# Kernel tuning notes

Hardware: AMD Instinct MI355X
Metric: run time of the kernel (lower is better)

The kernel has to match this reference:

```python
import jax, jax.numpy as jnp
import numpy as np

DIM = 1024
N_HEADS = 16
HEAD_DIM = DIM // N_HEADS


def setup_inputs() -> dict:
    key = jax.random.key(0)
    ks = jax.random.split(key, 5)
    B, L = 2, 2048
    q = jax.random.normal(ks[0], (B, L, DIM), dtype=jnp.float32)
    # nn.Linear weights: shape [out_features, in_features], applied as x @ W.T
    scale = 1.0 / np.sqrt(DIM)
    Wq = jax.random.normal(ks[1], (DIM, DIM), dtype=jnp.float32) * scale
    Wk = jax.random.normal(ks[2], (DIM, DIM), dtype=jnp.float32) * scale
    Wv = jax.random.normal(ks[3], (DIM, DIM), dtype=jnp.float32) * scale
    Wo = jax.random.normal(ks[4], (DIM, DIM), dtype=jnp.float32) * scale
    return {"q": q, "Wq": Wq, "Wk": Wk, "Wv": Wv, "Wo": Wo}


def reference(q, Wq, Wk, Wv, Wo):
    B, L, _ = q.shape
    kv = q  # self-attention (kv=None path)
    # projections: x @ W.T, then split heads: b l (h d) -> b h l d
    def split_heads(x):
        return x.reshape(B, L, N_HEADS, HEAD_DIM).transpose(0, 2, 1, 3)
    qh = split_heads(q @ Wq.T)
    kh = split_heads(kv @ Wk.T)
    vh = split_heads(kv @ Wv.T)
    # scaled dot-product attention; scale = sqrt(head_dim)
    scores = jnp.einsum('bhid,bhjd->bhij', qh, kh) / jnp.sqrt(
        jnp.asarray(HEAD_DIM, dtype=qh.dtype))
    attn = jax.nn.softmax(scores, axis=-1)
    out = jnp.einsum('bhij,bhjd->bhid', attn, vh)
    # b h l d -> b l (h d)
    out = out.transpose(0, 2, 1, 3).reshape(B, L, DIM)
    return out @ Wo.T
```

## Files before the change

kernel.cpp:

```cpp
#include <hip/hip_runtime.h>


#define DIMN 1024
#define NH 16
#define HD 64
#define BB 2
#define LL 2048

typedef float f32x4 __attribute__((ext_vector_type(4)));
typedef short s16x8 __attribute__((ext_vector_type(8)));

#define QSCALE 0.18033688011112042f

static __device__ __forceinline__ unsigned short f2bf(float f) {
  unsigned u = __float_as_uint(f);
  u += 0x7fffu + ((u >> 16) & 1u);
  return (unsigned short)(u >> 16);
}
static __device__ __forceinline__ unsigned packbf2(float lo, float hi) {
  return (unsigned)f2bf(lo) | ((unsigned)f2bf(hi) << 16);
}
static __device__ __forceinline__ float xexp2(float x) {
#if __has_builtin(__builtin_amdgcn_exp2f)
  return __builtin_amdgcn_exp2f(x);
#else
  return exp2f(x);
#endif
}
static __device__ __forceinline__ s16x8 cvt8(float4 a, float4 b) {
  s16x8 r;
  r[0] = (short)f2bf(a.x); r[1] = (short)f2bf(a.y);
  r[2] = (short)f2bf(a.z); r[3] = (short)f2bf(a.w);
  r[4] = (short)f2bf(b.x); r[5] = (short)f2bf(b.y);
  r[6] = (short)f2bf(b.z); r[7] = (short)f2bf(b.w);
  return r;
}
static __device__ __forceinline__ void gld16(const unsigned short* g,
                                             unsigned short* l) {
#if __has_builtin(__builtin_amdgcn_global_load_lds)
  __builtin_amdgcn_global_load_lds(
      (const __attribute__((address_space(1))) void*)g,
      (__attribute__((address_space(3))) void*)l, 16, 0, 0);
#else
  ((uint4*)l)[threadIdx.x & 63] = ((const uint4*)g)[0];
#endif
}

static __device__ __forceinline__ int vpos(int s128) {
  return (s128 & 0x60) | ((s128 & 0x0C) << 1) | ((s128 & 0x10) >> 2) | (s128 & 3);
}

__global__ __launch_bounds__(256) void cvt_all(
    const float* __restrict__ X, const float* __restrict__ Wq,
    const float* __restrict__ Wk, const float* __restrict__ Wv,
    const float* __restrict__ Wo, unsigned short* __restrict__ out) {
  const int blk = blockIdx.x;
  const float* src;
  unsigned short* dst;
  size_t off;
  if (blk < 2048) {
    src = X; dst = out; off = (size_t)blk * 2048;
  } else {
    int s = (blk - 2048) >> 9;
    src = (s == 0) ? Wq : (s == 1) ? Wk : (s == 2) ? Wv : Wo;
    dst = out + ((size_t)1 << 22) + (size_t)s * (1u << 20);
    off = (size_t)((blk - 2048) & 511) * 2048;
  }
  size_t i = off + (size_t)threadIdx.x * 8;
  float4 v0 = *(const float4*)(src + i);
  float4 v1 = *(const float4*)(src + i + 4);
  uint4 o;
  o.x = packbf2(v0.x, v0.y); o.y = packbf2(v0.z, v0.w);
  o.z = packbf2(v1.x, v1.y); o.w = packbf2(v1.z, v1.w);
  *(uint4*)(dst + i) = o;
}

__global__ __launch_bounds__(256) void gemm_qkv(
    const unsigned short* __restrict__ Xb, const unsigned short* __restrict__ Wb,
    unsigned short* __restrict__ Qb, unsigned short* __restrict__ Kb,
    unsigned short* __restrict__ VT) {
  __shared__ __align__(16) unsigned short Al[128 * 32];
  __shared__ __align__(16) unsigned short Bl[128 * 32];
  const int m0 = blockIdx.x * 128;
  const int n0g = blockIdx.y * 128;
  const int sel = n0g >> 10;
  const int tid = threadIdx.x;
  const int w = tid >> 6, lane = tid & 63;
  const int c = lane & 15, quad = lane >> 4;
  const int wm = (w & 1) * 64, wn = (w >> 1) * 64;

  f32x4 zero = {0.f, 0.f, 0.f, 0.f};
  f32x4 acc[4][4];
#pragma unroll
  for (int i = 0; i < 4; ++i)
#pragma unroll
    for (int j = 0; j < 4; ++j) acc[i][j] = zero;

  const int srow = w * 32 + (lane >> 2);
  const int scol = (lane & 3) * 8;
  const unsigned short* gA = Xb + (size_t)(m0 + srow) * DIMN + scol;
  const unsigned short* gB = Wb + (size_t)(n0g + srow) * DIMN + scol;
  unsigned short* lA0 = Al + (w * 32) * 32;
  unsigned short* lA1 = Al + (w * 32 + 16) * 32;
  unsigned short* lB0 = Bl + (w * 32) * 32;
  unsigned short* lB1 = Bl + (w * 32 + 16) * 32;

  for (int k0 = 0; k0 < DIMN; k0 += 32) {
    __syncthreads();
    gld16(gA + k0, lA0);
    gld16(gA + k0 + 16 * DIMN, lA1);
    gld16(gB + k0, lB0);
    gld16(gB + k0 + 16 * DIMN, lB1);
    __syncthreads();
    s16x8 a[4], b[4];
#pragma unroll
    for (int i = 0; i < 4; ++i)
      a[i] = *(const s16x8*)&Al[(wm + i * 16 + c) * 32 + quad * 8];
#pragma unroll
    for (int j = 0; j < 4; ++j)
      b[j] = *(const s16x8*)&Bl[(wn + j * 16 + c) * 32 + quad * 8];
    if (sel != 2) {
#pragma unroll
      for (int i = 0; i < 4; ++i)
#pragma unroll
        for (int j = 0; j < 4; ++j)
          acc[i][j] = __builtin_amdgcn_mfma_f32_16x16x32_bf16(a[i], b[j], acc[i][j], 0, 0, 0);
    } else {
#pragma unroll
      for (int i = 0; i < 4; ++i)
#pragma unroll
        for (int j = 0; j < 4; ++j)
          acc[i][j] = __builtin_amdgcn_mfma_f32_16x16x32_bf16(b[j], a[i], acc[i][j], 0, 0, 0);
    }
  }

  const int n0 = n0g & 1023;
  if (sel != 2) {
    unsigned short* Out = (sel == 0) ? Qb : Kb;
    const float scale = (sel == 0) ? QSCALE : 1.0f;
#pragma unroll
    for (int i = 0; i < 4; ++i)
#pragma unroll
      for (int j = 0; j < 4; ++j)
#pragma unroll
        for (int r = 0; r < 4; ++r) {
          int row = m0 + wm + i * 16 + quad * 4 + r;
          int col = n0 + wn + j * 16 + c;
          Out[(((size_t)(row >> 11) * NH + (col >> 6)) * LL + (row & 2047)) * HD + (col & 63)] =
              f2bf(acc[i][j][r] * scale);
        }
  } else {
#pragma unroll
    for (int i = 0; i < 4; ++i) {
#pragma unroll
      for (int j = 0; j < 4; ++j)
#pragma unroll
        for (int r = 0; r < 4; ++r) {
          int n = n0 + wn + j * 16 + quad * 4 + r;
          int sp = vpos(wm + i * 16 + c);
          int m = m0 + sp;
          int bi = (m0 + wm) >> 11;
          VT[(((size_t)bi * NH + (n >> 6)) * HD + (n & 63)) * LL + (m & 2047)] =
              f2bf(acc[i][j][r]);
        }
    }
  }
}

__global__ __launch_bounds__(256) void gemm_o(
    const unsigned short* __restrict__ A, const unsigned short* __restrict__ Wob,
    float* __restrict__ Out) {
  __shared__ __align__(16) unsigned short Al[128 * 32];
  __shared__ __align__(16) unsigned short Bl[64 * 32];
  const int m0 = blockIdx.x * 128;
  const int n0 = blockIdx.y * 64;
  const int tid = threadIdx.x;
  const int w = tid >> 6, lane = tid & 63;
  const int c = lane & 15, quad = lane >> 4;
  const int wm = (w & 1) * 64, wn = (w >> 1) * 32;

  f32x4 zero = {0.f, 0.f, 0.f, 0.f};
  f32x4 acc[4][2];
#pragma unroll
  for (int i = 0; i < 4; ++i)
#pragma unroll
    for (int j = 0; j < 2; ++j) acc[i][j] = zero;

  const int srow = w * 32 + (lane >> 2);
  const int brow = w * 16 + (lane >> 2);
  const int scol = (lane & 3) * 8;
  const unsigned short* gA = A + (size_t)(m0 + srow) * DIMN + scol;
  const unsigned short* gB = Wob + (size_t)(n0 + brow) * DIMN + scol;
  unsigned short* lA0 = Al + (w * 32) * 32;
  unsigned short* lA1 = Al + (w * 32 + 16) * 32;
  unsigned short* lB0 = Bl + (w * 16) * 32;

  for (int k0 = 0; k0 < DIMN; k0 += 32) {
    __syncthreads();
    gld16(gA + k0, lA0);
    gld16(gA + k0 + 16 * DIMN, lA1);
    gld16(gB + k0, lB0);
    __syncthreads();
    s16x8 a[4], b[2];
#pragma unroll
    for (int i = 0; i < 4; ++i)
      a[i] = *(const s16x8*)&Al[(wm + i * 16 + c) * 32 + quad * 8];
#pragma unroll
    for (int j = 0; j < 2; ++j)
      b[j] = *(const s16x8*)&Bl[(wn + j * 16 + c) * 32 + quad * 8];
#pragma unroll
    for (int i = 0; i < 4; ++i)
#pragma unroll
      for (int j = 0; j < 2; ++j)
        acc[i][j] = __builtin_amdgcn_mfma_f32_16x16x32_bf16(a[i], b[j], acc[i][j], 0, 0, 0);
  }

#pragma unroll
  for (int i = 0; i < 4; ++i)
#pragma unroll
    for (int j = 0; j < 2; ++j)
#pragma unroll
      for (int r = 0; r < 4; ++r)
        Out[(size_t)(m0 + wm + i * 16 + quad * 4 + r) * DIMN + n0 + wn + j * 16 + c] =
            acc[i][j][r];
}

__global__ __launch_bounds__(512) void attn6(
    const unsigned short* __restrict__ Qb, const unsigned short* __restrict__ Kb,
    const unsigned short* __restrict__ VT, unsigned short* __restrict__ AO) {
  __shared__ __align__(16) unsigned short Kl[2 * 128 * 64];
  __shared__ __align__(16) unsigned short Vtl[2 * 64 * 128];

  const int bh = blockIdx.y;
  const int tid = threadIdx.x;
  const int w = tid >> 6, lane = tid & 63;
  const int c = lane & 15, quad = lane >> 4;
  const int q0 = blockIdx.x * 128 + w * 16;

  const unsigned short* Qh = Qb + (size_t)bh * LL * HD;
  const unsigned short* Kh = Kb + (size_t)bh * LL * HD;
  const unsigned short* Vh = VT + (size_t)bh * HD * LL;

  s16x8 qf0 = *(const s16x8*)(Qh + (size_t)(q0 + c) * HD + quad * 8);
  s16x8 qf1 = *(const s16x8*)(Qh + (size_t)(q0 + c) * HD + 32 + quad * 8);

  f32x4 zero = {0.f, 0.f, 0.f, 0.f};
  f32x4 o[4];
  float lsum = 0.f;
#pragma unroll
  for (int dc = 0; dc < 4; ++dc) o[dc] = zero;

  const int l8 = lane >> 3, p8 = lane & 7;
  const unsigned short* gK = Kh + (size_t)(w * 16 + l8) * HD + ((p8 ^ l8) * 8);
  const int l16 = lane >> 4, p16 = lane & 15;
  const int vr0 = w * 8 + l16;
  const int vr1 = w * 8 + 4 + l16;
  const unsigned short* gV0 = Vh + (size_t)vr0 * LL + ((p16 ^ (vr0 & 15)) * 8);
  const unsigned short* gV1 = Vh + (size_t)vr1 * LL + ((p16 ^ (vr1 & 15)) * 8);

  const int kpa = (quad ^ (c & 7)) * 8;
  const int kpb = ((quad + 4) ^ (c & 7)) * 8;

#define STAGE(buf, k0)                                                        \
  do {                                                                        \
    unsigned short* lK_ = Kl + (buf) * (128 * 64) + (w * 16) * 64;            \
    unsigned short* lV_ = Vtl + (buf) * (64 * 128) + (w * 8) * 128;           \
    gld16(gK + (size_t)(k0) * HD, lK_);                                       \
    gld16(gK + (size_t)((k0) + 8) * HD, lK_ + 8 * 64);                        \
    gld16(gV0 + (k0), lV_);                                                   \
    gld16(gV1 + (k0), lV_ + 4 * 128);                                         \
  } while (0)

  STAGE(0, 0);

  for (int it = 0; it < LL / 128; ++it) {
    __syncthreads();
    if (it + 1 < LL / 128) STAGE((it + 1) & 1, (it + 1) * 128);
    const unsigned short* Kt = Kl + (it & 1) * (128 * 64);
    const unsigned short* Vt = Vtl + (it & 1) * (64 * 128);

#pragma unroll
    for (int g = 0; g < 2; ++g) {
      f32x4 s[4];
#pragma unroll
      for (int t4 = 0; t4 < 4; ++t4) {
        const unsigned short* kr = Kt + ((g * 4 + t4) * 16 + c) * 64;
        s16x8 kfa = *(const s16x8*)(kr + kpa);
        s16x8 kfb = *(const s16x8*)(kr + kpb);
        s[t4] = __builtin_amdgcn_mfma_f32_16x16x32_bf16(kfa, qf0, zero, 0, 0, 0);
        s[t4] = __builtin_amdgcn_mfma_f32_16x16x32_bf16(kfb, qf1, s[t4], 0, 0, 0);
      }
      float p[4][4];
      float acc_l = 0.f;
#pragma unroll
      for (int t4 = 0; t4 < 4; ++t4)
#pragma unroll
        for (int r = 0; r < 4; ++r) {
          float e = xexp2(s[t4][r]);
          p[t4][r] = e;
          acc_l += e;
        }
      lsum += acc_l;
#pragma unroll
      for (int kh = 0; kh < 2; ++kh) {
        const int kk = g * 2 + kh;
        unsigned pu[4];
        pu[0] = __builtin_amdgcn_perm(__float_as_uint(p[2 * kh][1]),
                                      __float_as_uint(p[2 * kh][0]), 0x07060302u);
        pu[1] = __builtin_amdgcn_perm(__float_as_uint(p[2 * kh][3]),
                                      __float_as_uint(p[2 * kh][2]), 0x07060302u);
        pu[2] = __builtin_amdgcn_perm(__float_as_uint(p[2 * kh + 1][1]),
                                      __float_as_uint(p[2 * kh + 1][0]), 0x07060302u);
        pu[3] = __builtin_amdgcn_perm(__float_as_uint(p[2 * kh + 1][3]),
                                      __float_as_uint(p[2 * kh + 1][2]), 0x07060302u);
        s16x8 pf = *(const s16x8*)pu;
#pragma unroll
        for (int dc = 0; dc < 4; ++dc) {
          s16x8 vf = *(const s16x8*)(Vt + (dc * 16 + c) * 128 + (((kk * 4 + quad) ^ c) * 8));
          o[dc] = __builtin_amdgcn_mfma_f32_16x16x32_bf16(vf, pf, o[dc], 0, 0, 0);
        }
      }
    }
  }
#undef STAGE

  const int bi = bh >> 4, h = bh & 15;
  float l = lsum;
  l += __shfl_xor(l, 16);
  l += __shfl_xor(l, 32);
  float inv = 1.0f / l;
  unsigned short* dst = AO + ((size_t)bi * LL + q0 + c) * DIMN + h * HD + quad * 4;
#pragma unroll
  for (int dc = 0; dc < 4; ++dc) {
    uint2 st;
    st.x = packbf2(o[dc][0] * inv, o[dc][1] * inv);
    st.y = packbf2(o[dc][2] * inv, o[dc][3] * inv);
    *(uint2*)(dst + dc * 16) = st;
  }
}

__global__ __launch_bounds__(64) void qkv_proj_f(
    const float* __restrict__ X, const float* __restrict__ Wq,
    const float* __restrict__ Wk, const float* __restrict__ Wv,
    unsigned short* __restrict__ Qb, unsigned short* __restrict__ Kb,
    unsigned short* __restrict__ VT) {
  const int m0 = blockIdx.x * 64;
  const int n0g = blockIdx.y * 64;
  const int sel = n0g >> 10;
  const int n0 = n0g & 1023;
  const float* W = (sel == 0) ? Wq : (sel == 1) ? Wk : Wv;
  const int lane = threadIdx.x;
  const int c = lane & 15, quad = lane >> 4;

  f32x4 zero = {0.f, 0.f, 0.f, 0.f};
  f32x4 acc[4][4];
#pragma unroll
  for (int i = 0; i < 4; ++i)
#pragma unroll
    for (int j = 0; j < 4; ++j) acc[i][j] = zero;

  const float* ab = X + (size_t)(m0 + c) * DIMN + quad * 8;
  const float* bb = W + (size_t)(n0 + c) * DIMN + quad * 8;

  for (int k0 = 0; k0 < DIMN; k0 += 32) {
    s16x8 a[4], b[4];
#pragma unroll
    for (int i = 0; i < 4; ++i) {
      const float* pp = ab + i * 16 * DIMN + k0;
      a[i] = cvt8(*(const float4*)pp, *(const float4*)(pp + 4));
    }
#pragma unroll
    for (int j = 0; j < 4; ++j) {
      const float* pp = bb + j * 16 * DIMN + k0;
      b[j] = cvt8(*(const float4*)pp, *(const float4*)(pp + 4));
    }
    if (sel != 2) {
#pragma unroll
      for (int i = 0; i < 4; ++i)
#pragma unroll
        for (int j = 0; j < 4; ++j)
          acc[i][j] = __builtin_amdgcn_mfma_f32_16x16x32_bf16(a[i], b[j], acc[i][j], 0, 0, 0);
    } else {
#pragma unroll
      for (int i = 0; i < 4; ++i)
#pragma unroll
        for (int j = 0; j < 4; ++j)
          acc[i][j] = __builtin_amdgcn_mfma_f32_16x16x32_bf16(b[j], a[i], acc[i][j], 0, 0, 0);
    }
  }

  if (sel != 2) {
    unsigned short* Out = (sel == 0) ? Qb : Kb;
    const float scale = (sel == 0) ? QSCALE : 1.0f;
#pragma unroll
    for (int i = 0; i < 4; ++i)
#pragma unroll
      for (int j = 0; j < 4; ++j)
#pragma unroll
        for (int r = 0; r < 4; ++r) {
          int row = m0 + i * 16 + quad * 4 + r;
          int nl = n0 + j * 16 + c;
          int bi = row >> 11, li = row & 2047;
          int h = nl >> 6, d = nl & 63;
          Out[(((size_t)bi * NH + h) * LL + li) * HD + d] = f2bf(acc[i][j][r] * scale);
        }
  } else {
#pragma unroll
    for (int i = 0; i < 4; ++i) {
#pragma unroll
      for (int j = 0; j < 4; ++j)
#pragma unroll
        for (int r = 0; r < 4; ++r) {
          int n = n0 + j * 16 + quad * 4 + r;
          int s128 = (m0 & 64) + i * 16 + c;
          int m = (m0 & ~127) + vpos(s128);
          int h = n >> 6, d = n & 63;
          int bi = m0 >> 11;
          VT[(((size_t)bi * NH + h) * HD + d) * LL + (m & 2047)] = f2bf(acc[i][j][r]);
        }
    }
  }
}

__global__ __launch_bounds__(64) void o_proj_f(
    const unsigned short* __restrict__ A, const float* __restrict__ Wo,
    float* __restrict__ Out) {
  const int m0 = blockIdx.x * 64, n0 = blockIdx.y * 64;
  const int lane = threadIdx.x;
  const int c = lane & 15, quad = lane >> 4;

  f32x4 zero = {0.f, 0.f, 0.f, 0.f};
  f32x4 acc[4][4];
#pragma unroll
  for (int i = 0; i < 4; ++i)
#pragma unroll
    for (int j = 0; j < 4; ++j) acc[i][j] = zero;

  const unsigned short* ab = A + (size_t)(m0 + c) * DIMN + quad * 8;
  const float* bb = Wo + (size_t)(n0 + c) * DIMN + quad * 8;

  for (int k0 = 0; k0 < DIMN; k0 += 32) {
    s16x8 a[4], b[4];
#pragma unroll
    for (int i = 0; i < 4; ++i) a[i] = *(const s16x8*)(ab + i * 16 * DIMN + k0);
#pragma unroll
    for (int j = 0; j < 4; ++j) {
      const float* pp = bb + j * 16 * DIMN + k0;
      b[j] = cvt8(*(const float4*)pp, *(const float4*)(pp + 4));
    }
#pragma unroll
    for (int i = 0; i < 4; ++i)
#pragma unroll
      for (int j = 0; j < 4; ++j)
        acc[i][j] = __builtin_amdgcn_mfma_f32_16x16x32_bf16(a[i], b[j], acc[i][j], 0, 0, 0);
  }

#pragma unroll
  for (int i = 0; i < 4; ++i)
#pragma unroll
    for (int j = 0; j < 4; ++j)
#pragma unroll
      for (int r = 0; r < 4; ++r)
        Out[(size_t)(m0 + i * 16 + quad * 4 + r) * DIMN + n0 + j * 16 + c] = acc[i][j][r];
}

extern "C" void kernel_launch(void* const* d_in, const int* in_sizes, int n_in,
                              void* d_out, int out_size, void* d_ws, size_t ws_size,
                              hipStream_t stream) {
  const float* X = (const float*)d_in[0];
  const float* Wq = (const float*)d_in[1];
  const float* Wk = (const float*)d_in[2];
  const float* Wv = (const float*)d_in[3];
  const float* Wo = (const float*)d_in[4];
  float* Out = (float*)d_out;

  const size_t M1 = (size_t)1 << 20;
  unsigned short* ws16 = (unsigned short*)d_ws;

  if (ws_size >= (size_t)48 * 1024 * 1024) {
    unsigned short* Xb = ws16;
    unsigned short* Wb = ws16 + 4 * M1;
    unsigned short* Qb = ws16 + 8 * M1;
    unsigned short* Kb = ws16 + 12 * M1;
    unsigned short* VT = ws16 + 16 * M1;
    unsigned short* AO = ws16 + 20 * M1;
    cvt_all<<<4096, 256, 0, stream>>>(X, Wq, Wk, Wv, Wo, ws16);
    gemm_qkv<<<dim3(32, 24), 256, 0, stream>>>(Xb, Wb, Qb, Kb, VT);
    attn6<<<dim3(LL / 128, BB * NH), 512, 0, stream>>>(Qb, Kb, VT, AO);
    gemm_o<<<dim3(32, 16), 256, 0, stream>>>(AO, Wb + 3 * M1, Out);
  } else {
    unsigned short* Qb = ws16;
    unsigned short* Kb = ws16 + 4 * M1;
    unsigned short* VT = ws16 + 8 * M1;
    unsigned short* AO = ws16 + 12 * M1;
    qkv_proj_f<<<dim3(64, 48), 64, 0, stream>>>(X, Wq, Wk, Wv, Qb, Kb, VT);
    attn6<<<dim3(LL / 128, BB * NH), 512, 0, stream>>>(Qb, Kb, VT, AO);
    o_proj_f<<<dim3(64, 16), 64, 0, stream>>>(AO, Wo, Out);
  }
}
```

Before: 187.2 us.

## Double-buffer LDS in projection GEMMs, swizzle tiles, vectorize epilogue stores

```diff
diff --git a/kernel.cpp b/kernel.cpp
--- a/kernel.cpp
+++ b/kernel.cpp
@@ -79,8 +79,8 @@
     const unsigned short* __restrict__ Xb, const unsigned short* __restrict__ Wb,
     unsigned short* __restrict__ Qb, unsigned short* __restrict__ Kb,
     unsigned short* __restrict__ VT) {
-  __shared__ __align__(16) unsigned short Al[128 * 32];
-  __shared__ __align__(16) unsigned short Bl[128 * 32];
+  __shared__ __align__(16) unsigned short Al[2][128 * 32];
+  __shared__ __align__(16) unsigned short Bl[2][128 * 32];
   const int m0 = blockIdx.x * 128;
   const int n0g = blockIdx.y * 128;
   const int sel = n0g >> 10;
@@ -97,72 +97,84 @@
     for (int j = 0; j < 4; ++j) acc[i][j] = zero;
 
   const int srow = w * 32 + (lane >> 2);
-  const int scol = (lane & 3) * 8;
+  const int ksw = ((lane >> 2) ^ (lane >> 4)) & 3;
+  const int scol = ((lane & 3) ^ ksw) * 8;
   const unsigned short* gA = Xb + (size_t)(m0 + srow) * DIMN + scol;
   const unsigned short* gB = Wb + (size_t)(n0g + srow) * DIMN + scol;
-  unsigned short* lA0 = Al + (w * 32) * 32;
-  unsigned short* lA1 = Al + (w * 32 + 16) * 32;
-  unsigned short* lB0 = Bl + (w * 32) * 32;
-  unsigned short* lB1 = Bl + (w * 32 + 16) * 32;
-
-  for (int k0 = 0; k0 < DIMN; k0 += 32) {
+
+  const int kc = (c ^ (c >> 2)) & 3;
+  const int rda = (quad ^ kc) * 8;
+
+#define STAGEQ(buf, k0)                                      \
+  do {                                                       \
+    gld16(gA + (k0), &Al[buf][(w * 32) * 32]);               \
+    gld16(gA + (k0) + 16 * DIMN, &Al[buf][(w * 32 + 16) * 32]); \
+    gld16(gB + (k0), &Bl[buf][(w * 32) * 32]);               \
+    gld16(gB + (k0) + 16 * DIMN, &Bl[buf][(w * 32 + 16) * 32]); \
+  } while (0)
+
+  STAGEQ(0, 0);
+  for (int kt = 0; kt < DIMN / 32; ++kt) {
     __syncthreads();
-    gld16(gA + k0, lA0);
-    gld16(gA + k0 + 16 * DIMN, lA1);
-    gld16(gB + k0, lB0);
-    gld16(gB + k0 + 16 * DIMN, lB1);
-    __syncthreads();
+    if (kt + 1 < DIMN / 32) STAGEQ((kt + 1) & 1, (kt + 1) * 32);
+    const unsigned short* At = Al[kt & 1];
+    const unsigned short* Bt = Bl[kt & 1];
     s16x8 a[4], b[4];
 #pragma unroll
     for (int i = 0; i < 4; ++i)
-      a[i] = *(const s16x8*)&Al[(wm + i * 16 + c) * 32 + quad * 8];
+      a[i] = *(const s16x8*)&At[(wm + i * 16 + c) * 32 + rda];
 #pragma unroll
     for (int j = 0; j < 4; ++j)
-      b[j] = *(const s16x8*)&Bl[(wn + j * 16 + c) * 32 + quad * 8];
+      b[j] = *(const s16x8*)&Bt[(wn + j * 16 + c) * 32 + rda];
     if (sel != 2) {
+#pragma unroll
+      for (int i = 0; i < 4; ++i)
+#pragma unroll
+        for (int j = 0; j < 4; ++j)
+          acc[i][j] = __builtin_amdgcn_mfma_f32_16x16x32_bf16(b[j], a[i], acc[i][j], 0, 0, 0);
+    } else {
 #pragma unroll
       for (int i = 0; i < 4; ++i)
 #pragma unroll
         for (int j = 0; j < 4; ++j)
           acc[i][j] = __builtin_amdgcn_mfma_f32_16x16x32_bf16(a[i], b[j], acc[i][j], 0, 0, 0);
-    } else {
-#pragma unroll
-      for (int i = 0; i < 4; ++i)
-#pragma unroll
-        for (int j = 0; j < 4; ++j)
-          acc[i][j] = __builtin_amdgcn_mfma_f32_16x16x32_bf16(b[j], a[i], acc[i][j], 0, 0, 0);
-    }
-  }
+    }
+  }
+#undef STAGEQ
 
   const int n0 = n0g & 1023;
   if (sel != 2) {
     unsigned short* Out = (sel == 0) ? Qb : Kb;
     const float scale = (sel == 0) ? QSCALE : 1.0f;
-#pragma unroll
-    for (int i = 0; i < 4; ++i)
-#pragma unroll
-      for (int j = 0; j < 4; ++j)
-#pragma unroll
-        for (int r = 0; r < 4; ++r) {
-          int row = m0 + wm + i * 16 + quad * 4 + r;
-          int col = n0 + wn + j * 16 + c;
-          Out[(((size_t)(row >> 11) * NH + (col >> 6)) * LL + (row & 2047)) * HD + (col & 63)] =
-              f2bf(acc[i][j][r] * scale);
-        }
+    const int bi = (m0 + wm) >> 11;
+#pragma unroll
+    for (int i = 0; i < 4; ++i) {
+      const int li = (m0 + wm + i * 16 + c) & 2047;
+#pragma unroll
+      for (int j = 0; j < 4; ++j) {
+        const int nq = n0 + wn + j * 16 + quad * 4;
+        const int h = nq >> 6, d = nq & 63;
+        uint2 st;
+        st.x = packbf2(acc[i][j][0] * scale, acc[i][j][1] * scale);
+        st.y = packbf2(acc[i][j][2] * scale, acc[i][j][3] * scale);
+        *(uint2*)&Out[(((size_t)bi * NH + h) * LL + li) * HD + d] = st;
+      }
+    }
   } else {
+    const int bi = m0 >> 11;
+    const int mlo = m0 & 2047;
 #pragma unroll
     for (int i = 0; i < 4; ++i) {
-#pragma unroll
-      for (int j = 0; j < 4; ++j)
-#pragma unroll
-        for (int r = 0; r < 4; ++r) {
-          int n = n0 + wn + j * 16 + quad * 4 + r;
-          int sp = vpos(wm + i * 16 + c);
-          int m = m0 + sp;
-          int bi = (m0 + wm) >> 11;
-          VT[(((size_t)bi * NH + (n >> 6)) * HD + (n & 63)) * LL + (m & 2047)] =
-              f2bf(acc[i][j][r]);
-        }
+      const int pos = mlo + vpos(wm + i * 16 + quad * 4);
+#pragma unroll
+      for (int j = 0; j < 4; ++j) {
+        const int nv = n0 + wn + j * 16 + c;
+        const int h = nv >> 6, d = nv & 63;
+        uint2 st;
+        st.x = packbf2(acc[i][j][0], acc[i][j][1]);
+        st.y = packbf2(acc[i][j][2], acc[i][j][3]);
+        *(uint2*)&VT[(((size_t)bi * NH + h) * HD + d) * LL + pos] = st;
+      }
     }
   }
 }
@@ -170,8 +182,8 @@
 __global__ __launch_bounds__(256) void gemm_o(
     const unsigned short* __restrict__ A, const unsigned short* __restrict__ Wob,
     float* __restrict__ Out) {
-  __shared__ __align__(16) unsigned short Al[128 * 32];
-  __shared__ __align__(16) unsigned short Bl[64 * 32];
+  __shared__ __align__(16) unsigned short Al[2][128 * 32];
+  __shared__ __align__(16) unsigned short Bl[2][64 * 32];
   const int m0 = blockIdx.x * 128;
   const int n0 = blockIdx.y * 64;
   const int tid = threadIdx.x;
@@ -188,32 +200,41 @@
 
   const int srow = w * 32 + (lane >> 2);
   const int brow = w * 16 + (lane >> 2);
-  const int scol = (lane & 3) * 8;
+  const int ksw = ((lane >> 2) ^ (lane >> 4)) & 3;
+  const int scol = ((lane & 3) ^ ksw) * 8;
   const unsigned short* gA = A + (size_t)(m0 + srow) * DIMN + scol;
   const unsigned short* gB = Wob + (size_t)(n0 + brow) * DIMN + scol;
-  unsigned short* lA0 = Al + (w * 32) * 32;
-  unsigned short* lA1 = Al + (w * 32 + 16) * 32;
-  unsigned short* lB0 = Bl + (w * 16) * 32;
-
-  for (int k0 = 0; k0 < DIMN; k0 += 32) {
+
+  const int kc = (c ^ (c >> 2)) & 3;
+  const int rda = (quad ^ kc) * 8;
+
+#define STAGEO(buf, k0)                                      \
+  do {                                                       \
+    gld16(gA + (k0), &Al[buf][(w * 32) * 32]);               \
+    gld16(gA + (k0) + 16 * DIMN, &Al[buf][(w * 32 + 16) * 32]); \
+    gld16(gB + (k0), &Bl[buf][(w * 16) * 32]);               \
+  } while (0)
+
+  STAGEO(0, 0);
+  for (int kt = 0; kt < DIMN / 32; ++kt) {
     __syncthreads();
-    gld16(gA + k0, lA0);
-    gld16(gA + k0 + 16 * DIMN, lA1);
-    gld16(gB + k0, lB0);
-    __syncthreads();
+    if (kt + 1 < DIMN / 32) STAGEO((kt + 1) & 1, (kt + 1) * 32);
+    const unsigned short* At = Al[kt & 1];
+    const unsigned short* Bt = Bl[kt & 1];
     s16x8 a[4], b[2];
 #pragma unroll
     for (int i = 0; i < 4; ++i)
-      a[i] = *(const s16x8*)&Al[(wm + i * 16 + c) * 32 + quad * 8];
+      a[i] = *(const s16x8*)&At[(wm + i * 16 + c) * 32 + rda];
 #pragma unroll
     for (int j = 0; j < 2; ++j)
-      b[j] = *(const s16x8*)&Bl[(wn + j * 16 + c) * 32 + quad * 8];
+      b[j] = *(const s16x8*)&Bt[(wn + j * 16 + c) * 32 + rda];
 #pragma unroll
     for (int i = 0; i < 4; ++i)
 #pragma unroll
       for (int j = 0; j < 2; ++j)
         acc[i][j] = __builtin_amdgcn_mfma_f32_16x16x32_bf16(a[i], b[j], acc[i][j], 0, 0, 0);
   }
+#undef STAGEO
 
 #pragma unroll
   for (int i = 0; i < 4; ++i)
```

Result: slower. 201.0 us (+7.4%).
